# Optimization experiments

Measured on AMD Instinct MI355X. Metric: run time of the kernel, lower is better.

Reference implementation:

```python
import jax, jax.numpy as jnp
import numpy as np

EPS = 1e-14
B, S, DIN, DOUT = 8, 2048, 1024, 1024


def setup_inputs() -> dict:
    key = jax.random.key(0)
    ks = jax.random.split(key, 10)
    xs = jax.random.normal(ks[0], (B, S, DIN), dtype=jnp.float32)
    # binary keep-mask over key positions (float, as in the torch code)
    mask = (jax.random.uniform(ks[1], (B, S)) < 0.9).astype(jnp.float32)
    w = 0.02
    Wk = jax.random.normal(ks[2], (DIN, DOUT), dtype=jnp.float32) * w
    bk = jnp.zeros((DOUT,), dtype=jnp.float32)
    Wq = jax.random.normal(ks[3], (DIN, DOUT), dtype=jnp.float32) * w
    bq = jnp.zeros((DOUT,), dtype=jnp.float32)
    Wv = jax.random.normal(ks[4], (DIN, DOUT), dtype=jnp.float32) * w
    bv = jnp.zeros((DOUT,), dtype=jnp.float32)
    Wl = jax.random.normal(ks[5], (DOUT, DOUT), dtype=jnp.float32) * w
    bl = jnp.zeros((DOUT,), dtype=jnp.float32)
    return {"xs": xs, "mask": mask, "Wk": Wk, "bk": bk, "Wq": Wq, "bq": bq,
            "Wv": Wv, "bv": bv, "Wl": Wl, "bl": bl}


def reference(xs, mask, Wk, bk, Wq, bq, Wv, bv, Wl, bl):
    k = xs @ Wk + bk          # [b, s, d]
    q = xs @ Wq + bq          # [b, s, d]
    v = xs @ Wv + bv          # [b, s, d]
    # qk[b,i,j] = <k_i, q_j>  (einsum 'bsd,bde->bse' with q transposed)
    qk = jnp.einsum('bid,bjd->bij', k, q)
    # softmax over axis 1 (key rows), temperature = in_dim
    a = jax.nn.softmax(qk / xs.shape[-1], axis=1)
    # mask.repeat(1,s).view(b,s,s) tiles mask along rows -> mask columns j
    a = a * mask[:, None, :] + EPS
    # 'bij,bik->bik' contracts only j: row-sum of a scales v elementwise
    rowsum = jnp.sum(a, axis=2)              # [b, s]
    attn = rowsum[:, :, None] * v            # [b, s, d]
    out = jax.nn.leaky_relu(attn @ Wl + bl, negative_slope=0.01)
    return out
```

## Files before the change

kernel.cpp:

```cpp
#include <hip/hip_runtime.h>

#define B_ 8
#define S_ 2048
#define DIN_ 1024
#define DOUT_ 1024

using bf16 = __bf16;
using bf16x4 = __attribute__((ext_vector_type(4))) bf16;
using bf16x8 = __attribute__((ext_vector_type(8))) bf16;
using f32x4  = __attribute__((ext_vector_type(4))) float;


__global__ __launch_bounds__(256) void cast_k(const float* __restrict__ in,
                                              bf16* __restrict__ out, long n) {
  long i = ((long)blockIdx.x * blockDim.x + threadIdx.x) * 4;
  long stride = (long)gridDim.x * blockDim.x * 4;
  for (; i < n; i += stride) {
    float4 v = *(const float4*)(in + i);
    bf16x4 o = { (bf16)v.x, (bf16)v.y, (bf16)v.z, (bf16)v.w };
    *(bf16x4*)(out + i) = o;
  }
}

__global__ __launch_bounds__(1024) void transpose_cast_k(const float* __restrict__ in,
                                                         bf16* __restrict__ out) {
  __shared__ float tile[32][33];
  int x = blockIdx.x * 32 + threadIdx.x;
  int y = blockIdx.y * 32 + threadIdx.y;
  tile[threadIdx.y][threadIdx.x] = in[y * 1024 + x];
  __syncthreads();
  int xo = blockIdx.y * 32 + threadIdx.x;
  int yo = blockIdx.x * 32 + threadIdx.y;
  out[yo * 1024 + xo] = (bf16)tile[threadIdx.x][threadIdx.y];
}

__global__ __launch_bounds__(256) void rowdot_k(const float* __restrict__ W,
                                                const float* __restrict__ v,
                                                float* __restrict__ out, int cols) {
  int row = blockIdx.x * 4 + (threadIdx.x >> 6);
  int lane = threadIdx.x & 63;
  float s = 0.f;
  const float* p = W + (long)row * cols;
  for (int c = lane; c < cols; c += 64) s += p[c] * v[c];
#pragma unroll
  for (int o = 32; o; o >>= 1) s += __shfl_down(s, o);
  if (!lane) out[row] = s;
}

__global__ __launch_bounds__(256) void dot1_k(const float* __restrict__ a,
                                              const float* __restrict__ b,
                                              float* __restrict__ out, int n) {
  __shared__ float sm[256];
  float s = 0.f;
  for (int i = threadIdx.x; i < n; i += 256) s += a[i] * b[i];
  sm[threadIdx.x] = s;
  __syncthreads();
  for (int o = 128; o; o >>= 1) {
    if (threadIdx.x < o) sm[threadIdx.x] += sm[threadIdx.x + o];
    __syncthreads();
  }
  if (!threadIdx.x) out[0] = sm[0];
}

__global__ __launch_bounds__(256) void colmat_k(const float* __restrict__ Wl,
                                                const float* __restrict__ bv,
                                                float* __restrict__ c2) {
  int e = blockIdx.x * 256 + threadIdx.x;
  float s = 0.f;
  for (int f = 0; f < 1024; f++) s += bv[f] * Wl[f * 1024 + e];
  c2[e] = s;
}

__global__ __launch_bounds__(256) void alphabeta_k(const float* __restrict__ xs,
                                                   const float* __restrict__ kb,
                                                   const float* __restrict__ qb,
                                                   float* __restrict__ al,
                                                   float* __restrict__ be) {
  int row = blockIdx.x * 4 + (threadIdx.x >> 6);
  int lane = threadIdx.x & 63;
  const float* x = xs + (long)row * DIN_;
  float sa = 0.f, sb = 0.f;
  for (int c = lane; c < DIN_; c += 64) {
    float xv = x[c];
    sa += xv * kb[c];
    sb += xv * qb[c];
  }
#pragma unroll
  for (int o = 32; o; o >>= 1) { sa += __shfl_down(sa, o); sb += __shfl_down(sb, o); }
  if (!lane) { al[row] = sa; be[row] = sb; }
}

__global__ __launch_bounds__(256) void rowsum_k(const bf16* __restrict__ E,
                                                const float* __restrict__ mask,
                                                const float* __restrict__ csum,
                                                float* __restrict__ rs) {
  int row = blockIdx.x * 4 + (threadIdx.x >> 6);
  int lane = threadIdx.x & 63;
  int b = row >> 11;
  const bf16* p = E + (long)row * S_;
  const float* mb = mask + b * S_;
  const float* cb = csum + b * S_;
  float s = 0.f;
  for (int j = lane * 4; j < S_; j += 256) {
    bf16x4 ev = *(const bf16x4*)(p + j);
    float4 mv = *(const float4*)(mb + j);
    float4 cv = *(const float4*)(cb + j);
    s += (float)ev[0] * mv.x / cv.x + (float)ev[1] * mv.y / cv.y +
         (float)ev[2] * mv.z / cv.z + (float)ev[3] * mv.w / cv.w;
  }
#pragma unroll
  for (int o = 32; o; o >>= 1) s += __shfl_down(s, o);
  if (!lane) rs[row] = s + 2.048e-11f;
}

__device__ __forceinline__ void gld16(const bf16* g, bf16* l) {
  __builtin_amdgcn_global_load_lds(
      (__attribute__((address_space(1))) void*)const_cast<bf16*>(g),
      (__attribute__((address_space(3))) void*)l, 16, 0, 0);
}

__global__ __launch_bounds__(256) void gemm_bt(
    const bf16* __restrict__ A, const bf16* __restrict__ B,
    int M, int N, int K, void* __restrict__ C) {
  __shared__ __align__(16) bf16 As[128 * 32];
  __shared__ __align__(16) bf16 Bs[128 * 32];
  const int tid = threadIdx.x;
  const int wid = tid >> 6, lane = tid & 63;
  const int bm0 = blockIdx.y * 128, bn0 = blockIdx.x * 128;
  const int mb = (wid >> 1) * 64, nb = (wid & 1) * 64;
  const int fr = lane & 15, ko = (lane >> 4) * 8;

  f32x4 acc[4][4] = {};

  const int srow = wid * 32 + (lane >> 2);
  const int scol = (lane & 3) * 8;
  const bf16* gA = A + (long)(bm0 + srow) * K + scol;
  const bf16* gB = B + (long)(bn0 + srow) * K + scol;
  bf16* lA = As + wid * 32 * 32;
  bf16* lB = Bs + wid * 32 * 32;

  for (int k0 = 0; k0 < K; k0 += 32) {
    gld16(gA + k0, lA);
    gld16(gA + 16 * K + k0, lA + 16 * 32);
    gld16(gB + k0, lB);
    gld16(gB + 16 * K + k0, lB + 16 * 32);
    __syncthreads();
    bf16x8 af[4], bfr[4];
#pragma unroll
    for (int m = 0; m < 4; m++)
      af[m] = *(const bf16x8*)(As + (mb + m * 16 + fr) * 32 + ko);
#pragma unroll
    for (int n = 0; n < 4; n++)
      bfr[n] = *(const bf16x8*)(Bs + (nb + n * 16 + fr) * 32 + ko);
#pragma unroll
    for (int m = 0; m < 4; m++)
#pragma unroll
      for (int n = 0; n < 4; n++)
        acc[m][n] = __builtin_amdgcn_mfma_f32_16x16x32_bf16(af[m], bfr[n], acc[m][n], 0, 0, 0);
    __syncthreads();
  }

  const int ci = (lane >> 4) * 4;
  bf16* Cp = (bf16*)C;
#pragma unroll
  for (int m = 0; m < 4; m++) {
    const int rb = bm0 + mb + m * 16 + ci;
#pragma unroll
    for (int n = 0; n < 4; n++) {
      const int cb = bn0 + nb + n * 16 + fr;
#pragma unroll
      for (int r = 0; r < 4; r++)
        Cp[(long)(rb + r) * N + cb] = (bf16)acc[m][n][r];
    }
  }
}


template <int EPI>
__global__ __launch_bounds__(512, 1) void gemm3(
    const bf16* __restrict__ A, const bf16* __restrict__ B,
    int M, int N, int K, long sA, long sB, long sC, void* __restrict__ C,
    const float* __restrict__ e0, const float* __restrict__ e1,
    const float* __restrict__ e2, float* __restrict__ e3) {
  __shared__ __align__(16) bf16 sm[3 * 24576];
  const int tid = threadIdx.x;
  const int wid = tid >> 6, lane = tid & 63;
  const int z = blockIdx.z;
  A += (long)z * sA;
  B += (long)z * sB;
  const int bm0 = blockIdx.y * 256, bn0 = blockIdx.x * 128;
  const int wm = wid >> 1, wn = wid & 1;
  const int NT = K >> 6;

  const int lrow = lane >> 3;
  const int lseg = (lane & 7) ^ lrow;
  const bf16* gA = A + (long)(bm0 + wid * 32 + lrow) * K + lseg * 8;
  const bf16* gB = B + (long)(bn0 + wid * 16 + lrow) * K + lseg * 8;

  f32x4 acc[4][4] = {};

  auto STAGE = [&](int buf, int t) {
    bf16* lA = sm + buf * 24576 + wid * 2048;
    bf16* lB = sm + buf * 24576 + 16384 + wid * 1024;
    const bf16* ga = gA + t * 64;
    const bf16* gb = gB + t * 64;
#pragma unroll
    for (int l = 0; l < 4; l++) gld16(ga + (long)l * 8 * K, lA + l * 512);
#pragma unroll
    for (int l = 0; l < 2; l++) gld16(gb + (long)l * 8 * K, lB + l * 512);
  };

  STAGE(0, 0);
  if (NT > 1) STAGE(1, 1);
  asm volatile("s_waitcnt vmcnt(6)" ::: "memory");
  __builtin_amdgcn_s_barrier();

  const int fr = lane & 15;
  const int rowA0 = wm * 64 + fr;
  const int rowB0 = wn * 64 + fr;
  const int seg0 = lane >> 4;

  for (int t = 0; t < NT; ++t) {
    const bf16* Ab = sm + (t % 3) * 24576;
    const bf16* Bb = Ab + 16384;
    if (t + 2 < NT) STAGE((t + 2) % 3, t + 2);
#pragma unroll
    for (int kh = 0; kh < 2; kh++) {
      bf16x8 a[4], b[4];
#pragma unroll
      for (int m = 0; m < 4; m++) {
        const int row = rowA0 + m * 16;
        const int s = (seg0 + 4 * kh) ^ (row & 7);
        a[m] = *(const bf16x8*)(Ab + row * 64 + s * 8);
      }
#pragma unroll
      for (int n = 0; n < 4; n++) {
        const int row = rowB0 + n * 16;
        const int s = (seg0 + 4 * kh) ^ (row & 7);
        b[n] = *(const bf16x8*)(Bb + row * 64 + s * 8);
      }
      __builtin_amdgcn_s_setprio(1);
#pragma unroll
      for (int m = 0; m < 4; m++)
#pragma unroll
        for (int n = 0; n < 4; n++)
          acc[m][n] = __builtin_amdgcn_mfma_f32_16x16x32_bf16(a[m], b[n], acc[m][n], 0, 0, 0);
      __builtin_amdgcn_s_setprio(0);
    }
    if (t < NT - 1) {
      if (t + 2 < NT) asm volatile("s_waitcnt vmcnt(6)" ::: "memory");
      else            asm volatile("s_waitcnt vmcnt(0)" ::: "memory");
      __builtin_amdgcn_s_barrier();
    }
  }

  const int ci = (lane >> 4) * 4;
  const int cj = fr;
  if constexpr (EPI == 0 || EPI == 1) {
    bf16* Cp = (bf16*)C + (long)z * sC;
    float gam = (EPI == 1) ? e2[0] : 0.f;
    float colp[4] = {0.f, 0.f, 0.f, 0.f};
#pragma unroll
    for (int m = 0; m < 4; m++) {
      const int rb = bm0 + wm * 64 + m * 16 + ci;
#pragma unroll
      for (int n = 0; n < 4; n++) {
        const int cb = bn0 + wn * 64 + n * 16 + cj;
#pragma unroll
        for (int r = 0; r < 4; r++) {
          float v = acc[m][n][r];
          if constexpr (EPI == 1) {
            v = __expf((v + e0[z * M + rb + r] + e1[z * N + cb] + gam) * (1.f / 1024.f));
            colp[n] += v;
          }
          Cp[(long)(rb + r) * N + cb] = (bf16)v;
        }
      }
    }
    if constexpr (EPI == 1) {
#pragma unroll
      for (int n = 0; n < 4; n++) {
        float s = colp[n];
        s += __shfl_xor(s, 16);
        s += __shfl_xor(s, 32);
        if (lane < 16)
          atomicAdd(&e3[(long)z * N + bn0 + wn * 64 + n * 16 + cj], s);
      }
    }
  } else {
    float* Cp = (float*)C;
#pragma unroll
    for (int m = 0; m < 4; m++) {
      const int rb = bm0 + wm * 64 + m * 16 + ci;
#pragma unroll
      for (int n = 0; n < 4; n++) {
        const int cb = bn0 + wn * 64 + n * 16 + cj;
#pragma unroll
        for (int r = 0; r < 4; r++) {
          float v = e0[rb + r] * (acc[m][n][r] + e1[cb]) + e2[cb];
          v = v < 0.f ? 0.01f * v : v;
          Cp[(long)(rb + r) * N + cb] = v;
        }
      }
    }
  }
}


extern "C" void kernel_launch(void* const* d_in, const int* in_sizes, int n_in,
                              void* d_out, int out_size, void* d_ws, size_t ws_size,
                              hipStream_t stream) {
  const float* xs   = (const float*)d_in[0];
  const float* mask = (const float*)d_in[1];
  const float* Wk   = (const float*)d_in[2];
  const float* bk   = (const float*)d_in[3];
  const float* Wq   = (const float*)d_in[4];
  const float* bq   = (const float*)d_in[5];
  const float* Wv   = (const float*)d_in[6];
  const float* bv   = (const float*)d_in[7];
  const float* Wl   = (const float*)d_in[8];
  const float* bl   = (const float*)d_in[9];
  float* out = (float*)d_out;

  char* ws = (char*)d_ws;
  size_t off = 0;
  auto alloc = [&](size_t bytes) -> void* {
    void* p = ws + off;
    off += (bytes + 255) & ~(size_t)255;
    return p;
  };
  bf16* xs_bf = (bf16*)alloc((size_t)B_ * S_ * DIN_ * 2);
  bf16* t_bf  = (bf16*)alloc((size_t)B_ * S_ * DOUT_ * 2);
  bf16* Wk_bf = (bf16*)alloc((size_t)DIN_ * DOUT_ * 2);
  bf16* Wq_bf = (bf16*)alloc((size_t)DIN_ * DOUT_ * 2);
  bf16* Wv_bf = (bf16*)alloc((size_t)DIN_ * DOUT_ * 2);
  bf16* Wl_t  = (bf16*)alloc((size_t)DIN_ * DOUT_ * 2);
  bf16* Mt    = (bf16*)alloc((size_t)DIN_ * DOUT_ * 2);
  bf16* W2t   = (bf16*)alloc((size_t)DIN_ * DOUT_ * 2);
  float* kb    = (float*)alloc(DIN_ * 4);
  float* qb    = (float*)alloc(DIN_ * 4);
  float* c2    = (float*)alloc(DOUT_ * 4);
  float* gma   = (float*)alloc(256);
  float* alpha = (float*)alloc((size_t)B_ * S_ * 4);
  float* beta  = (float*)alloc((size_t)B_ * S_ * 4);
  float* csum  = (float*)alloc((size_t)B_ * S_ * 4);
  float* rs    = (float*)alloc((size_t)B_ * S_ * 4);
  size_t Eb = (size_t)B_ * S_ * S_ * 2;
  bf16* E = (off + Eb <= ws_size) ? (bf16*)alloc(Eb) : (bf16*)d_out;

  cast_k<<<4096, 256, 0, stream>>>(xs, xs_bf, (long)B_ * S_ * DIN_);
  cast_k<<<1024, 256, 0, stream>>>(Wk, Wk_bf, (long)DIN_ * DOUT_);
  cast_k<<<1024, 256, 0, stream>>>(Wq, Wq_bf, (long)DIN_ * DOUT_);
  cast_k<<<1024, 256, 0, stream>>>(Wv, Wv_bf, (long)DIN_ * DOUT_);
  transpose_cast_k<<<dim3(32, 32), dim3(32, 32), 0, stream>>>(Wl, Wl_t);

  rowdot_k<<<256, 256, 0, stream>>>(Wk, bq, kb, DOUT_);
  rowdot_k<<<256, 256, 0, stream>>>(Wq, bk, qb, DOUT_);
  dot1_k<<<1, 256, 0, stream>>>(bk, bq, gma, DOUT_);
  colmat_k<<<4, 256, 0, stream>>>(Wl, bv, c2);
  alphabeta_k<<<4096, 256, 0, stream>>>(xs, kb, qb, alpha, beta);

  gemm_bt<<<dim3(8, 8, 1), 256, 0, stream>>>(Wq_bf, Wk_bf, 1024, 1024, 1024, Mt);
  gemm_bt<<<dim3(8, 8, 1), 256, 0, stream>>>(Wl_t, Wv_bf, 1024, 1024, 1024, W2t);
  gemm3<0><<<dim3(8, 64, 1), 512, 0, stream>>>(xs_bf, Mt, B_ * S_, 1024, 1024,
                                               0, 0, 0, t_bf, nullptr, nullptr, nullptr, nullptr);
  hipMemsetAsync(csum, 0, (size_t)B_ * S_ * 4, stream);
  gemm3<1><<<dim3(16, 8, 8), 512, 0, stream>>>(t_bf, xs_bf, S_, S_, 1024,
                                               (long)S_ * DIN_, (long)S_ * DIN_,
                                               (long)S_ * S_, E, alpha, beta, gma, csum);
  rowsum_k<<<4096, 256, 0, stream>>>(E, mask, csum, rs);
  gemm3<2><<<dim3(8, 64, 1), 512, 0, stream>>>(xs_bf, W2t, B_ * S_, 1024, 1024,
                                               0, 0, 0, out, rs, c2, bl, nullptr);
}
```

Before: 488.0 us.

## Enlarge gemm3 tile to 256x256 with double buffering; split colmat over K

The main GEMM kernel goes from 256x128 to 256x256 block tiles, with each wave computing a 128x64 sub-tile (8x4 MFMA accumulators). The LDS pipeline drops from three stages to two, with plain __syncthreads in place of the vmcnt-based waits. This is meant to raise arithmetic intensity and cut global/LDS traffic per FLOP, at the cost of more registers, half as many blocks and less latency hiding. Separately, colmat_k is split over the reduction dimension with atomicAdd so it uses more blocks, and the memsets are moved to the start of the launch sequence.

```diff
diff --git a/kernel.cpp b/kernel.cpp
--- a/kernel.cpp
+++ b/kernel.cpp
@@ -66,9 +66,11 @@
                                                 const float* __restrict__ bv,
                                                 float* __restrict__ c2) {
   int e = blockIdx.x * 256 + threadIdx.x;
+  int f0 = blockIdx.y * 32;
   float s = 0.f;
-  for (int f = 0; f < 1024; f++) s += bv[f] * Wl[f * 1024 + e];
-  c2[e] = s;
+#pragma unroll 8
+  for (int f = f0; f < f0 + 32; f++) s += bv[f] * Wl[(long)f * 1024 + e];
+  atomicAdd(&c2[e], s);
 }
 
 __global__ __launch_bounds__(256) void alphabeta_k(const float* __restrict__ xs,
@@ -182,76 +184,72 @@
     int M, int N, int K, long sA, long sB, long sC, void* __restrict__ C,
     const float* __restrict__ e0, const float* __restrict__ e1,
     const float* __restrict__ e2, float* __restrict__ e3) {
-  __shared__ __align__(16) bf16 sm[3 * 24576];
+  __shared__ __align__(16) bf16 sm[2 * 32768];
   const int tid = threadIdx.x;
   const int wid = tid >> 6, lane = tid & 63;
   const int z = blockIdx.z;
   A += (long)z * sA;
   B += (long)z * sB;
-  const int bm0 = blockIdx.y * 256, bn0 = blockIdx.x * 128;
-  const int wm = wid >> 1, wn = wid & 1;
+  const int bm0 = blockIdx.y * 256, bn0 = blockIdx.x * 256;
+  const int wm = wid >> 2, wn = wid & 3;
   const int NT = K >> 6;
 
   const int lrow = lane >> 3;
   const int lseg = (lane & 7) ^ lrow;
   const bf16* gA = A + (long)(bm0 + wid * 32 + lrow) * K + lseg * 8;
-  const bf16* gB = B + (long)(bn0 + wid * 16 + lrow) * K + lseg * 8;
-
-  f32x4 acc[4][4] = {};
+  const bf16* gB = B + (long)(bn0 + wid * 32 + lrow) * K + lseg * 8;
+
+  f32x4 acc[8][4] = {};
 
   auto STAGE = [&](int buf, int t) {
-    bf16* lA = sm + buf * 24576 + wid * 2048;
-    bf16* lB = sm + buf * 24576 + 16384 + wid * 1024;
+    bf16* lA = sm + buf * 32768 + wid * 2048;
+    bf16* lB = sm + buf * 32768 + 16384 + wid * 2048;
     const bf16* ga = gA + t * 64;
     const bf16* gb = gB + t * 64;
 #pragma unroll
     for (int l = 0; l < 4; l++) gld16(ga + (long)l * 8 * K, lA + l * 512);
 #pragma unroll
-    for (int l = 0; l < 2; l++) gld16(gb + (long)l * 8 * K, lB + l * 512);
+    for (int l = 0; l < 4; l++) gld16(gb + (long)l * 8 * K, lB + l * 512);
   };
 
   STAGE(0, 0);
-  if (NT > 1) STAGE(1, 1);
-  asm volatile("s_waitcnt vmcnt(6)" ::: "memory");
-  __builtin_amdgcn_s_barrier();
+  __syncthreads();
 
   const int fr = lane & 15;
-  const int rowA0 = wm * 64 + fr;
-  const int rowB0 = wn * 64 + fr;
   const int seg0 = lane >> 4;
 
   for (int t = 0; t < NT; ++t) {
-    const bf16* Ab = sm + (t % 3) * 24576;
+    const bf16* Ab = sm + (t & 1) * 32768;
     const bf16* Bb = Ab + 16384;
-    if (t + 2 < NT) STAGE((t + 2) % 3, t + 2);
+    if (t + 1 < NT) STAGE((t + 1) & 1, t + 1);
 #pragma unroll
     for (int kh = 0; kh < 2; kh++) {
-      bf16x8 a[4], b[4];
-#pragma unroll
-      for (int m = 0; m < 4; m++) {
-        const int row = rowA0 + m * 16;
-        const int s = (seg0 + 4 * kh) ^ (row & 7);
-        a[m] = *(const bf16x8*)(Ab + row * 64 + s * 8);
-      }
+      bf16x8 b[4];
 #pragma unroll
       for (int n = 0; n < 4; n++) {
-        const int row = rowB0 + n * 16;
+        const int row = wn * 64 + n * 16 + fr;
         const int s = (seg0 + 4 * kh) ^ (row & 7);
         b[n] = *(const bf16x8*)(Bb + row * 64 + s * 8);
       }
-      __builtin_amdgcn_s_setprio(1);
-#pragma unroll
-      for (int m = 0; m < 4; m++)
-#pragma unroll
-        for (int n = 0; n < 4; n++)
-          acc[m][n] = __builtin_amdgcn_mfma_f32_16x16x32_bf16(a[m], b[n], acc[m][n], 0, 0, 0);
-      __builtin_amdgcn_s_setprio(0);
-    }
-    if (t < NT - 1) {
-      if (t + 2 < NT) asm volatile("s_waitcnt vmcnt(6)" ::: "memory");
-      else            asm volatile("s_waitcnt vmcnt(0)" ::: "memory");
-      __builtin_amdgcn_s_barrier();
-    }
+#pragma unroll
+      for (int mh = 0; mh < 2; mh++) {
+        bf16x8 a[4];
+#pragma unroll
+        for (int m = 0; m < 4; m++) {
+          const int row = wm * 128 + mh * 64 + m * 16 + fr;
+          const int s = (seg0 + 4 * kh) ^ (row & 7);
+          a[m] = *(const bf16x8*)(Ab + row * 64 + s * 8);
+        }
+        __builtin_amdgcn_s_setprio(1);
+#pragma unroll
+        for (int m = 0; m < 4; m++)
+#pragma unroll
+          for (int n = 0; n < 4; n++)
+            acc[mh * 4 + m][n] = __builtin_amdgcn_mfma_f32_16x16x32_bf16(a[m], b[n], acc[mh * 4 + m][n], 0, 0, 0);
+        __builtin_amdgcn_s_setprio(0);
+      }
+    }
+    if (t + 1 < NT) __syncthreads();
   }
 
   const int ci = (lane >> 4) * 4;
@@ -261,8 +259,8 @@
     float gam = (EPI == 1) ? e2[0] : 0.f;
     float colp[4] = {0.f, 0.f, 0.f, 0.f};
 #pragma unroll
-    for (int m = 0; m < 4; m++) {
-      const int rb = bm0 + wm * 64 + m * 16 + ci;
+    for (int m = 0; m < 8; m++) {
+      const int rb = bm0 + wm * 128 + m * 16 + ci;
 #pragma unroll
       for (int n = 0; n < 4; n++) {
         const int cb = bn0 + wn * 64 + n * 16 + cj;
@@ -290,8 +288,8 @@
   } else {
     float* Cp = (float*)C;
 #pragma unroll
-    for (int m = 0; m < 4; m++) {
-      const int rb = bm0 + wm * 64 + m * 16 + ci;
+    for (int m = 0; m < 8; m++) {
+      const int rb = bm0 + wm * 128 + m * 16 + ci;
 #pragma unroll
       for (int n = 0; n < 4; n++) {
         const int cb = bn0 + wn * 64 + n * 16 + cj;
@@ -348,6 +346,9 @@
   size_t Eb = (size_t)B_ * S_ * S_ * 2;
   bf16* E = (off + Eb <= ws_size) ? (bf16*)alloc(Eb) : (bf16*)d_out;
 
+  hipMemsetAsync(csum, 0, (size_t)B_ * S_ * 4, stream);
+  hipMemsetAsync(c2, 0, DOUT_ * 4, stream);
+
   cast_k<<<4096, 256, 0, stream>>>(xs, xs_bf, (long)B_ * S_ * DIN_);
   cast_k<<<1024, 256, 0, stream>>>(Wk, Wk_bf, (long)DIN_ * DOUT_);
   cast_k<<<1024, 256, 0, stream>>>(Wq, Wq_bf, (long)DIN_ * DOUT_);
@@ -357,18 +358,17 @@
   rowdot_k<<<256, 256, 0, stream>>>(Wk, bq, kb, DOUT_);
   rowdot_k<<<256, 256, 0, stream>>>(Wq, bk, qb, DOUT_);
   dot1_k<<<1, 256, 0, stream>>>(bk, bq, gma, DOUT_);
-  colmat_k<<<4, 256, 0, stream>>>(Wl, bv, c2);
+  colmat_k<<<dim3(4, 32), 256, 0, stream>>>(Wl, bv, c2);
   alphabeta_k<<<4096, 256, 0, stream>>>(xs, kb, qb, alpha, beta);
 
   gemm_bt<<<dim3(8, 8, 1), 256, 0, stream>>>(Wq_bf, Wk_bf, 1024, 1024, 1024, Mt);
   gemm_bt<<<dim3(8, 8, 1), 256, 0, stream>>>(Wl_t, Wv_bf, 1024, 1024, 1024, W2t);
-  gemm3<0><<<dim3(8, 64, 1), 512, 0, stream>>>(xs_bf, Mt, B_ * S_, 1024, 1024,
+  gemm3<0><<<dim3(4, 64, 1), 512, 0, stream>>>(xs_bf, Mt, B_ * S_, 1024, 1024,
                                                0, 0, 0, t_bf, nullptr, nullptr, nullptr, nullptr);
-  hipMemsetAsync(csum, 0, (size_t)B_ * S_ * 4, stream);
-  gemm3<1><<<dim3(16, 8, 8), 512, 0, stream>>>(t_bf, xs_bf, S_, S_, 1024,
-                                               (long)S_ * DIN_, (long)S_ * DIN_,
-                                               (long)S_ * S_, E, alpha, beta, gma, csum);
+  gemm3<1><<<dim3(8, 8, 8), 512, 0, stream>>>(t_bf, xs_bf, S_, S_, 1024,
+                                              (long)S_ * DIN_, (long)S_ * DIN_,
+                                              (long)S_ * S_, E, alpha, beta, gma, csum);
   rowsum_k<<<4096, 256, 0, stream>>>(E, mask, csum, rs);
-  gemm3<2><<<dim3(8, 64, 1), 512, 0, stream>>>(xs_bf, W2t, B_ * S_, 1024, 1024,
+  gemm3<2><<<dim3(4, 64, 1), 512, 0, stream>>>(xs_bf, W2t, B_ * S_, 1024, 1024,
                                                0, 0, 0, out, rs, c2, bl, nullptr);
 }
```

Result: faster. 400.0 us (-18.0%).
